# Performance work log

Hardware: AMD Instinct MI355X
Metric: run time of the kernel (lower is better)

Reference implementation:

```python
import jax, jax.numpy as jnp
import numpy as np

P = 16          # patch size
NH = 12         # num heads
DH = 64         # head dim
C = 768         # embed dim
DEPTH = 12
HID = 3072      # mlp hidden = 4*C
EPS = 1e-6


def _ln(x, g, b):
    m = x.mean(-1, keepdims=True)
    v = ((x - m) ** 2).mean(-1, keepdims=True)
    return (x - m) / jnp.sqrt(v + EPS) * g + b


def _rope_tables(seq_len, dim):
    inv_freq = 1.0 / (10000.0 ** (jnp.arange(0, dim, 2, dtype=jnp.float32) / dim))
    freqs = jnp.arange(seq_len, dtype=jnp.float32)[:, None] * inv_freq[None, :]  # [S, dim/2]
    emb = jnp.concatenate([freqs, freqs], axis=-1)  # [S, dim] (concat layout, as in source)
    return jnp.cos(emb), jnp.sin(emb)


def _apply_rope(q, k, cos, sin):
    def rot(t):  # interleaved rotate-half, exactly as torch source
        t1, t2 = t[..., ::2], t[..., 1::2]
        return jnp.stack([-t2, t1], axis=-1).reshape(t.shape)
    return q * cos + rot(q) * sin, k * cos + rot(k) * sin


def setup_inputs() -> dict:
    key = jax.random.key(0)
    ks = jax.random.split(key, 16)
    w = lambda k, shp: (jax.random.normal(k, shp, dtype=jnp.float32) * 0.02)
    inp = {
        "x": jax.random.normal(ks[0], (4, 6, 320, 320), dtype=jnp.float32),
        "conv_w": w(ks[1], (C, 3, P, P)),
        "conv_b": jnp.zeros((C,), jnp.float32),
        "ln1_g": jnp.ones((DEPTH, C), jnp.float32),
        "ln1_b": jnp.zeros((DEPTH, C), jnp.float32),
        "qkv_w": w(ks[2], (DEPTH, C, 3 * C)),
        "qkv_b": jnp.zeros((DEPTH, 3 * C), jnp.float32),
        "proj_w": w(ks[3], (DEPTH, C, C)),
        "proj_b": jnp.zeros((DEPTH, C), jnp.float32),
        "ln2_g": jnp.ones((DEPTH, C), jnp.float32),
        "ln2_b": jnp.zeros((DEPTH, C), jnp.float32),
        "fc1_w": w(ks[4], (DEPTH, C, HID)),
        "fc1_b": jnp.zeros((DEPTH, HID), jnp.float32),
        "fc2_w": w(ks[5], (DEPTH, HID, C)),
        "fc2_b": jnp.zeros((DEPTH, C), jnp.float32),
        "lnf_g": jnp.ones((C,), jnp.float32),
        "lnf_b": jnp.zeros((C,), jnp.float32),
    }
    return inp


def reference(x, conv_w, conv_b, ln1_g, ln1_b, qkv_w, qkv_b, proj_w, proj_b,
              ln2_g, ln2_b, fc1_w, fc1_b, fc2_w, fc2_b, lnf_g, lnf_b):
    B = x.shape[0]

    def embed(img):  # [B,3,H,W] -> [B, (H/P)*(W/P), C]
        y = jax.lax.conv_general_dilated(
            img, conv_w, window_strides=(P, P), padding="VALID",
            dimension_numbers=("NCHW", "OIHW", "NCHW")) + conv_b[None, :, None, None]
        b, c, hg, wg = y.shape
        return y.reshape(b, c, hg * wg).transpose(0, 2, 1)

    t = jnp.concatenate([embed(x[:, :3]), embed(x[:, 3:])], axis=1)  # [B,S,C], S=2*400=800
    S = t.shape[1]
    cos, sin = _rope_tables(S, DH)
    cos, sin = cos[None, None], sin[None, None]  # [1,1,S,DH]
    scale = DH ** -0.5

    def block(h, p):
        l1g, l1b, qw, qb, pw, pb, l2g, l2b, f1w, f1b, f2w, f2b = p
        y = _ln(h, l1g, l1b)
        qkv = (y @ qw + qb).reshape(B, S, 3, NH, DH).transpose(2, 0, 3, 1, 4)
        q, k, v = qkv[0], qkv[1], qkv[2]  # [B,NH,S,DH]
        q, k = _apply_rope(q, k, cos, sin)
        a = jax.nn.softmax(jnp.einsum("bhsd,bhtd->bhst", q, k) * scale, axis=-1)
        o = jnp.einsum("bhst,bhtd->bhsd", a, v).transpose(0, 2, 1, 3).reshape(B, S, C)
        h = h + (o @ pw + pb)
        y = _ln(h, l2g, l2b)
        h = h + (jax.nn.gelu(y @ f1w + f1b, approximate=False) @ f2w + f2b)
        return h, None

    params = (ln1_g, ln1_b, qkv_w, qkv_b, proj_w, proj_b,
              ln2_g, ln2_b, fc1_w, fc1_b, fc2_w, fc2_b)
    t, _ = jax.lax.scan(block, t, params)
    return _ln(t, lnf_g, lnf_b)
```

## Files before the change

### kernel.cpp

```cpp
#include <hip/hip_runtime.h>
#include <hip/hip_bf16.h>
#include <math.h>

#define S_LEN   800
#define SP_LEN  896
#define C_DIM   768
#define NHEAD   12
#define DHEAD   64
#define HID_DIM 3072
#define BATCH   4
#define NTOK    (BATCH * S_LEN)
#define DEPTH_N 12

using bf16x8 = __attribute__((ext_vector_type(8))) short;
using f32x4  = __attribute__((ext_vector_type(4))) float;

__device__ inline short f2bf(float x) {
    unsigned u = __builtin_bit_cast(unsigned, x);
    u += 0x7fff + ((u >> 16) & 1);
    return (short)(u >> 16);
}
__device__ inline float bf2f(short x) {
    unsigned u = ((unsigned)(unsigned short)x) << 16;
    return __builtin_bit_cast(float, u);
}

typedef const __attribute__((address_space(1))) void* gas_ptr;
typedef __attribute__((address_space(3))) void* las_ptr;
__device__ inline void async_copy16(const void* g, void* l) {
    __builtin_amdgcn_global_load_lds((gas_ptr)g, (las_ptr)l, 16, 0, 0);
}

__global__ __launch_bounds__(256)
void transpose_convert_kernel(const float* __restrict__ W, short* __restrict__ Wt,
                              int K, int N) {
    __shared__ float tile[32][33];
    int k0 = blockIdx.y * 32, n0 = blockIdx.x * 32;
    int tx = threadIdx.x & 31, ty = threadIdx.x >> 5;
#pragma unroll
    for (int i = ty; i < 32; i += 8)
        tile[i][tx] = W[(size_t)(k0 + i) * N + n0 + tx];
    __syncthreads();
#pragma unroll
    for (int i = ty; i < 32; i += 8)
        Wt[(size_t)(n0 + i) * K + k0 + tx] = f2bf(tile[tx][i]);
}

__global__ void convert_bf_kernel(const float* __restrict__ a, short* __restrict__ o, int n) {
    int i = blockIdx.x * 256 + threadIdx.x;
    if (i < n) o[i] = f2bf(a[i]);
}

__global__ void im2col_kernel(const float* __restrict__ x, short* __restrict__ A) {
    int idx = blockIdx.x * 256 + threadIdx.x;
    if (idx >= NTOK * 768) return;
    int kk = idx % 768;
    int s  = (idx / 768) % S_LEN;
    int b  = idx / (768 * S_LEN);
    int c  = kk / 256;
    int i  = (kk / 16) % 16;
    int j  = kk % 16;
    int half = s / 400, ss = s % 400;
    int hg = ss / 20, wg = ss % 20;
    int ch = half * 3 + c;
    A[idx] = f2bf(x[((size_t)(b * 6 + ch) * 320 + hg * 16 + i) * 320 + wg * 16 + j]);
}

template <int BN, bool GELU, bool RES, bool OBF>
__global__ __launch_bounds__(256)
void gemm_mfma(const short* __restrict__ A, const short* __restrict__ Bt,
               const float* __restrict__ bias, const float* __restrict__ res,
               void* __restrict__ Cout, int M, int N, int K) {
    constexpr int BM = 128, BK = 64;
    constexpr int TI = (BN == 128) ? 4 : 2;
    constexpr int TJ = 4;
    constexpr int ACALLS = BM * BK / (8 * 64);
    constexpr int BCALLS = BN * BK / (8 * 64);

    __shared__ __align__(16) short As[BM * BK];
    __shared__ __align__(16) short Bs[BN * BK];

    int tid = threadIdx.x;
    int w = tid >> 6, lane = tid & 63;
    int m0 = blockIdx.y * BM, n0 = blockIdx.x * BN;

    int wr = (BN == 128) ? (w >> 1) * 64 : w * 32;
    int wc = (BN == 128) ? (w & 1) * 64 : 0;

    f32x4 acc[TI][TJ];
#pragma unroll
    for (int i = 0; i < TI; ++i)
#pragma unroll
        for (int j = 0; j < TJ; ++j)
            acc[i][j] = (f32x4){0.f, 0.f, 0.f, 0.f};

    int lc = lane & 15, lq = lane >> 4;

    for (int k0 = 0; k0 < K; k0 += BK) {
#pragma unroll
        for (int j = w; j < ACALLS; j += 4) {
            int c = j * 64 + lane;
            int row = c >> 3, p = c & 7, q = p ^ (row & 7);
            async_copy16(A + (size_t)(m0 + row) * K + k0 + q * 8, As + j * 512);
        }
#pragma unroll
        for (int j = w; j < BCALLS; j += 4) {
            int c = j * 64 + lane;
            int row = c >> 3, p = c & 7, q = p ^ (row & 7);
            async_copy16(Bt + (size_t)(n0 + row) * K + k0 + q * 8, Bs + j * 512);
        }
        __syncthreads();

#pragma unroll
        for (int h = 0; h < 2; ++h) {
            bf16x8 afrag[TI], bfrag[TJ];
#pragma unroll
            for (int i = 0; i < TI; ++i) {
                int row = wr + i * 16 + lc;
                afrag[i] = *(const bf16x8*)(As + row * 64 + ((((h << 2) | lq)) ^ (row & 7)) * 8);
            }
#pragma unroll
            for (int j = 0; j < TJ; ++j) {
                int col = wc + j * 16 + lc;
                bfrag[j] = *(const bf16x8*)(Bs + col * 64 + ((((h << 2) | lq)) ^ (col & 7)) * 8);
            }
#pragma unroll
            for (int i = 0; i < TI; ++i)
#pragma unroll
                for (int j = 0; j < TJ; ++j)
                    acc[i][j] = __builtin_amdgcn_mfma_f32_16x16x32_bf16(
                        afrag[i], bfrag[j], acc[i][j], 0, 0, 0);
        }
        __syncthreads();
    }

    int rbase = lq * 4;
#pragma unroll
    for (int i = 0; i < TI; ++i)
#pragma unroll
        for (int j = 0; j < TJ; ++j)
#pragma unroll
            for (int r = 0; r < 4; ++r) {
                int m = m0 + wr + i * 16 + rbase + r;
                int n = n0 + wc + j * 16 + lc;
                float v = acc[i][j][r] + bias[n];
                if (RES) v += res[(size_t)m * N + n];
                if (GELU) v = 0.5f * v * (1.0f + erff(v * 0.70710678118654752f));
                if (OBF) ((short*)Cout)[(size_t)m * N + n] = f2bf(v);
                else     ((float*)Cout)[(size_t)m * N + n] = v;
            }
}

template <bool OBF>
__global__ __launch_bounds__(256)
void ln_kernel(const float* __restrict__ x, const float* __restrict__ g,
               const float* __restrict__ bta, void* __restrict__ yv) {
    int row = blockIdx.x;
    const float* xr = x + (size_t)row * C_DIM;
    int tid = threadIdx.x;

    float v0 = xr[tid], v1 = xr[tid + 256], v2 = xr[tid + 512];
    float s  = v0 + v1 + v2;
    float sq = v0 * v0 + v1 * v1 + v2 * v2;
#pragma unroll
    for (int off = 32; off; off >>= 1) {
        s  += __shfl_down(s, off);
        sq += __shfl_down(sq, off);
    }
    __shared__ float red1[4], red2[4];
    __shared__ float mean_s, rstd_s;
    int wv = tid / 64, lane = tid % 64;
    if (lane == 0) { red1[wv] = s; red2[wv] = sq; }
    __syncthreads();
    if (tid == 0) {
        float S1 = red1[0] + red1[1] + red1[2] + red1[3];
        float S2 = red2[0] + red2[1] + red2[2] + red2[3];
        float m = S1 / (float)C_DIM;
        float var = S2 / (float)C_DIM - m * m;
        mean_s = m;
        rstd_s = rsqrtf(var + 1e-6f);
    }
    __syncthreads();
    float m = mean_s, r = rstd_s;
    float o0 = (v0 - m) * r * g[tid]       + bta[tid];
    float o1 = (v1 - m) * r * g[tid + 256] + bta[tid + 256];
    float o2 = (v2 - m) * r * g[tid + 512] + bta[tid + 512];
    if (OBF) {
        short* yr = (short*)yv + (size_t)row * C_DIM;
        yr[tid] = f2bf(o0); yr[tid + 256] = f2bf(o1); yr[tid + 512] = f2bf(o2);
    } else {
        float* yr = (float*)yv + (size_t)row * C_DIM;
        yr[tid] = o0; yr[tid + 256] = o1; yr[tid + 512] = o2;
    }
}

__global__ __launch_bounds__(256)
void rope_qkv_kernel(const short* __restrict__ qkv, short* __restrict__ qb,
                     short* __restrict__ kb, short* __restrict__ vtb) {
    int st = blockIdx.x;
    int bh = blockIdx.y;
    int b = bh / NHEAD, h = bh % NHEAD;
    int s0 = st * 64;

    __shared__ __align__(16) short vlds[64][72];

    int tid = threadIdx.x;
    int sl = tid >> 2;
    int dc = (tid & 3) * 16;
    int s = s0 + sl;

    short qo[16], ko[16];
    if (s < S_LEN) {
        const short* base = qkv + ((size_t)(b * S_LEN + s)) * (3 * C_DIM) + h * DHEAD + dc;
        short qsh[16], ksh[16], vsh[16];
        *(bf16x8*)(qsh)     = *(const bf16x8*)(base);
        *(bf16x8*)(qsh + 8) = *(const bf16x8*)(base + 8);
        *(bf16x8*)(ksh)     = *(const bf16x8*)(base + C_DIM);
        *(bf16x8*)(ksh + 8) = *(const bf16x8*)(base + C_DIM + 8);
        *(bf16x8*)(vsh)     = *(const bf16x8*)(base + 2 * C_DIM);
        *(bf16x8*)(vsh + 8) = *(const bf16x8*)(base + 2 * C_DIM + 8);
        float qv[16], kv[16];
#pragma unroll
        for (int i = 0; i < 16; ++i) { qv[i] = bf2f(qsh[i]); kv[i] = bf2f(ksh[i]); }
#pragma unroll
        for (int i = 0; i < 16; ++i) {
            int d = dc + i;
            float ang = (float)s * exp2f(-(float)(d & 31) * 0.41524101186092029f);
            float c = cosf(ang), sn = sinf(ang);
            float sign = (i & 1) ? 1.0f : -1.0f;
            qo[i] = f2bf((qv[i] * c + sign * qv[i ^ 1] * sn) * 0.18033688011112042f);
            ko[i] = f2bf(kv[i] * c + sign * kv[i ^ 1] * sn);
        }
        *(bf16x8*)&vlds[sl][dc]     = *(bf16x8*)(vsh);
        *(bf16x8*)&vlds[sl][dc + 8] = *(bf16x8*)(vsh + 8);
    } else {
#pragma unroll
        for (int i = 0; i < 16; ++i) { qo[i] = 0; ko[i] = 0; vlds[sl][dc + i] = 0; }
    }
    {
        short* qd = qb + ((size_t)bh * SP_LEN + s) * DHEAD + dc;
        short* kd = kb + ((size_t)bh * SP_LEN + s) * DHEAD + dc;
        *(bf16x8*)(qd)     = *(bf16x8*)(qo);
        *(bf16x8*)(qd + 8) = *(bf16x8*)(qo + 8);
        *(bf16x8*)(kd)     = *(bf16x8*)(ko);
        *(bf16x8*)(kd + 8) = *(bf16x8*)(ko + 8);
    }
    __syncthreads();
    {
        int dr = tid >> 2, sc = (tid & 3) * 16;
        short vo[16];
#pragma unroll
        for (int i = 0; i < 16; ++i) vo[i] = vlds[sc + i][dr];
        short* vd = vtb + ((size_t)bh * DHEAD + dr) * SP_LEN + s0 + sc;
        *(bf16x8*)(vd)     = *(bf16x8*)(vo);
        *(bf16x8*)(vd + 8) = *(bf16x8*)(vo + 8);
    }
}

__global__ __launch_bounds__(256)
void attn_mfma_kernel(const short* __restrict__ qb, const short* __restrict__ kb,
                      const short* __restrict__ vtb, short* __restrict__ o) {
    int qt = blockIdx.x;
    int bh = blockIdx.y;
    int b = bh / NHEAD, h = bh % NHEAD;
    int m0 = qt * 64;

    __shared__ __align__(16) short Qs[64 * 64];
    __shared__ __align__(16) short Ks[128 * 64];
    __shared__ __align__(16) short Vts[64 * 128];
    __shared__ __align__(16) short Ps[64 * 136];

    int tid = threadIdx.x;
    int w = tid >> 6, lane = tid & 63;
    int lc = lane & 15, lq = lane >> 4;
    int kq = lq * 8;

    const short* qbase = qb + (size_t)bh * SP_LEN * DHEAD;
    const short* kbase = kb + (size_t)bh * SP_LEN * DHEAD;
    const short* vbase = vtb + (size_t)bh * DHEAD * SP_LEN;

    f32x4 oacc[4];
#pragma unroll
    for (int t = 0; t < 4; ++t) oacc[t] = (f32x4){0.f, 0.f, 0.f, 0.f};
    float mrow[4] = {-3.0e38f, -3.0e38f, -3.0e38f, -3.0e38f};
    float lrow[4] = {0.f, 0.f, 0.f, 0.f};

#pragma unroll
    for (int j = w; j < 8; j += 4) {
        int c = j * 64 + lane;
        int row = c >> 3, p = c & 7, q = p ^ (row & 7);
        async_copy16(qbase + (size_t)(m0 + row) * DHEAD + q * 8, Qs + j * 512);
    }

    for (int it = 0; it < 7; ++it) {
        int kt = it * 128;
#pragma unroll
        for (int j = w; j < 16; j += 4) {
            int c = j * 64 + lane;
            int row = c >> 3, p = c & 7, q = p ^ (row & 7);
            async_copy16(kbase + (size_t)(kt + row) * DHEAD + q * 8, Ks + j * 512);
        }
#pragma unroll
        for (int j = w; j < 16; j += 4) {
            int c = j * 64 + lane;
            int d = c >> 4, p = c & 15, sq = p ^ (d & 15);
            async_copy16(vbase + (size_t)d * SP_LEN + kt + sq * 8, Vts + j * 512);
        }
        __syncthreads();

        int nt = (it < 6) ? 8 : 2;

        int qrow = w * 16 + lc;
        bf16x8 aq0 = *(const bf16x8*)(Qs + qrow * 64 + ((lq) ^ (qrow & 7)) * 8);
        bf16x8 aq1 = *(const bf16x8*)(Qs + qrow * 64 + ((4 | lq) ^ (qrow & 7)) * 8);

        f32x4 sacc[8];
        for (int t = 0; t < nt; ++t) {
            int kr = t * 16 + lc;
            bf16x8 bk0 = *(const bf16x8*)(Ks + kr * 64 + ((lq) ^ (kr & 7)) * 8);
            bf16x8 bk1 = *(const bf16x8*)(Ks + kr * 64 + ((4 | lq) ^ (kr & 7)) * 8);
            f32x4 z = (f32x4){0.f, 0.f, 0.f, 0.f};
            z = __builtin_amdgcn_mfma_f32_16x16x32_bf16(aq0, bk0, z, 0, 0, 0);
            z = __builtin_amdgcn_mfma_f32_16x16x32_bf16(aq1, bk1, z, 0, 0, 0);
            sacc[t] = z;
        }

        float rmax[4];
#pragma unroll
        for (int r = 0; r < 4; ++r) {
            float m = sacc[0][r];
            for (int t = 1; t < nt; ++t) m = fmaxf(m, sacc[t][r]);
            rmax[r] = m;
        }
#pragma unroll
        for (int off = 1; off < 16; off <<= 1)
#pragma unroll
            for (int r = 0; r < 4; ++r)
                rmax[r] = fmaxf(rmax[r], __shfl_xor(rmax[r], off));

        float alpha[4], rsum[4] = {0.f, 0.f, 0.f, 0.f};
#pragma unroll
        for (int r = 0; r < 4; ++r) {
            float mnew = fmaxf(mrow[r], rmax[r]);
            alpha[r] = exp2f(mrow[r] - mnew);
            mrow[r] = mnew;
        }
        for (int t = 0; t < nt; ++t) {
#pragma unroll
            for (int r = 0; r < 4; ++r) {
                float p = exp2f(sacc[t][r] - mrow[r]);
                rsum[r] += p;
                Ps[(w * 16 + lq * 4 + r) * 136 + t * 16 + lc] = f2bf(p);
            }
        }
#pragma unroll
        for (int off = 1; off < 16; off <<= 1)
#pragma unroll
            for (int r = 0; r < 4; ++r)
                rsum[r] += __shfl_xor(rsum[r], off);
#pragma unroll
        for (int r = 0; r < 4; ++r) lrow[r] = lrow[r] * alpha[r] + rsum[r];
#pragma unroll
        for (int t = 0; t < 4; ++t)
#pragma unroll
            for (int r = 0; r < 4; ++r) oacc[t][r] *= alpha[r];

        int nk = (nt == 8) ? 4 : 1;
        for (int kstep = 0; kstep < nk; ++kstep) {
            bf16x8 ap = *(const bf16x8*)(Ps + (w * 16 + lc) * 136 + kstep * 32 + kq);
#pragma unroll
            for (int t = 0; t < 4; ++t) {
                int dr = t * 16 + lc;
                bf16x8 bv = *(const bf16x8*)(Vts + dr * 128 + ((((kstep << 2) | lq)) ^ (dr & 15)) * 8);
                oacc[t] = __builtin_amdgcn_mfma_f32_16x16x32_bf16(ap, bv, oacc[t], 0, 0, 0);
            }
        }
        __syncthreads();
    }

    float inv_l[4];
#pragma unroll
    for (int r = 0; r < 4; ++r) inv_l[r] = 1.0f / lrow[r];
#pragma unroll
    for (int t = 0; t < 4; ++t)
#pragma unroll
        for (int r = 0; r < 4; ++r) {
            int row = w * 16 + lq * 4 + r;
            int s = m0 + row;
            if (s < S_LEN) {
                int n = t * 16 + lc;
                o[((size_t)(b * S_LEN + s)) * C_DIM + h * DHEAD + n] = f2bf(oacc[t][r] * inv_l[r]);
            }
        }
}

extern "C" void kernel_launch(void* const* d_in, const int* in_sizes, int n_in,
                              void* d_out, int out_size, void* d_ws, size_t ws_size,
                              hipStream_t stream) {
    const float* x      = (const float*)d_in[0];
    const float* conv_w = (const float*)d_in[1];
    const float* conv_b = (const float*)d_in[2];
    const float* ln1_g  = (const float*)d_in[3];
    const float* ln1_b  = (const float*)d_in[4];
    const float* qkv_w  = (const float*)d_in[5];
    const float* qkv_b  = (const float*)d_in[6];
    const float* proj_w = (const float*)d_in[7];
    const float* proj_b = (const float*)d_in[8];
    const float* ln2_g  = (const float*)d_in[9];
    const float* ln2_b  = (const float*)d_in[10];
    const float* fc1_w  = (const float*)d_in[11];
    const float* fc1_b  = (const float*)d_in[12];
    const float* fc2_w  = (const float*)d_in[13];
    const float* fc2_b  = (const float*)d_in[14];
    const float* lnf_g  = (const float*)d_in[15];
    const float* lnf_b  = (const float*)d_in[16];

    const size_t NTC = (size_t)NTOK * C_DIM;
    const size_t HSD = (size_t)BATCH * NHEAD * SP_LEN * DHEAD;
    float* ws = (float*)d_ws;
    float* h       = ws;
    short* qkv_bf  = (short*)(h + NTC);
    short* qb      = qkv_bf + (size_t)NTOK * 3 * C_DIM;
    short* kb      = qb + HSD;
    short* vtb     = kb + HSD;
    short* y_bf    = vtb + HSD;
    short* big_bf  = y_bf + NTC;
    short* wbuf    = big_bf + (size_t)NTOK * HID_DIM;
    short* embed_wt = wbuf + (size_t)HID_DIM * C_DIM;

    convert_bf_kernel<<<(768 * 768 + 255) / 256, 256, 0, stream>>>(conv_w, embed_wt, 768 * 768);
    im2col_kernel<<<(NTOK * 768 + 255) / 256, 256, 0, stream>>>(x, big_bf);
    gemm_mfma<64, false, false, false><<<dim3(C_DIM / 64, NTOK / 128), 256, 0, stream>>>(
        big_bf, embed_wt, conv_b, nullptr, h, NTOK, C_DIM, C_DIM);

    for (int l = 0; l < DEPTH_N; ++l) {
        const float* l1g = ln1_g + (size_t)l * C_DIM;
        const float* l1b = ln1_b + (size_t)l * C_DIM;
        const float* qw  = qkv_w + (size_t)l * C_DIM * 3 * C_DIM;
        const float* qbs = qkv_b + (size_t)l * 3 * C_DIM;
        const float* pw  = proj_w + (size_t)l * C_DIM * C_DIM;
        const float* pb  = proj_b + (size_t)l * C_DIM;
        const float* l2g = ln2_g + (size_t)l * C_DIM;
        const float* l2b = ln2_b + (size_t)l * C_DIM;
        const float* f1w = fc1_w + (size_t)l * C_DIM * HID_DIM;
        const float* f1b = fc1_b + (size_t)l * HID_DIM;
        const float* f2w = fc2_w + (size_t)l * HID_DIM * C_DIM;
        const float* f2b = fc2_b + (size_t)l * C_DIM;

        ln_kernel<true><<<NTOK, 256, 0, stream>>>(h, l1g, l1b, y_bf);
        transpose_convert_kernel<<<dim3(3 * C_DIM / 32, C_DIM / 32), 256, 0, stream>>>(
            qw, wbuf, C_DIM, 3 * C_DIM);
        gemm_mfma<128, false, false, true><<<dim3(3 * C_DIM / 128, NTOK / 128), 256, 0, stream>>>(
            y_bf, wbuf, qbs, nullptr, qkv_bf, NTOK, 3 * C_DIM, C_DIM);

        rope_qkv_kernel<<<dim3(14, BATCH * NHEAD), 256, 0, stream>>>(qkv_bf, qb, kb, vtb);
        attn_mfma_kernel<<<dim3(13, BATCH * NHEAD), 256, 0, stream>>>(qb, kb, vtb, y_bf);

        transpose_convert_kernel<<<dim3(C_DIM / 32, C_DIM / 32), 256, 0, stream>>>(
            pw, wbuf, C_DIM, C_DIM);
        gemm_mfma<64, false, true, false><<<dim3(C_DIM / 64, NTOK / 128), 256, 0, stream>>>(
            y_bf, wbuf, pb, h, h, NTOK, C_DIM, C_DIM);

        ln_kernel<true><<<NTOK, 256, 0, stream>>>(h, l2g, l2b, y_bf);
        transpose_convert_kernel<<<dim3(HID_DIM / 32, C_DIM / 32), 256, 0, stream>>>(
            f1w, wbuf, C_DIM, HID_DIM);
        gemm_mfma<128, true, false, true><<<dim3(HID_DIM / 128, NTOK / 128), 256, 0, stream>>>(
            y_bf, wbuf, f1b, nullptr, big_bf, NTOK, HID_DIM, C_DIM);
        transpose_convert_kernel<<<dim3(C_DIM / 32, HID_DIM / 32), 256, 0, stream>>>(
            f2w, wbuf, HID_DIM, C_DIM);
        gemm_mfma<64, false, true, false><<<dim3(C_DIM / 64, NTOK / 128), 256, 0, stream>>>(
            big_bf, wbuf, f2b, h, h, NTOK, C_DIM, HID_DIM);
    }

    ln_kernel<false><<<NTOK, 256, 0, stream>>>(h, lnf_g, lnf_b, d_out);
}
```

Before: 2.803 ms.

## Add 256x256 pipelined MFMA GEMM for QKV/FC1 and batch weight transposes

Introduces a new 512-thread GEMM kernel with 256x256 output tiles, swizzled LDS layout, double-buffered async global-to-LDS loads and raised wave priority around the MFMA blocks. It is used for the QKV and FC1 projections to increase data reuse per tile. The four per-layer weight transpose/convert launches are merged into a single kernel writing to separate buffers, which removes launch overhead. In exchange, the large tiles give only about 117–156 blocks per GEMM, which may leave many CUs idle. The 128KB LDS use per block also limits occupancy, and the tail tile reads A rows past M, though those stores are guarded.

```diff
diff --git a/kernel.cpp b/kernel.cpp
--- a/kernel.cpp
+++ b/kernel.cpp
@@ -31,11 +31,17 @@
     __builtin_amdgcn_global_load_lds((gas_ptr)g, (las_ptr)l, 16, 0, 0);
 }
 
-__global__ __launch_bounds__(256)
-void transpose_convert_kernel(const float* __restrict__ W, short* __restrict__ Wt,
-                              int K, int N) {
+struct TP4 {
+    const float *qw, *pw, *f1, *f2;
+    short *wq, *wp, *w1, *w2;
+};
+
+template <int K, int N>
+__device__ __forceinline__ void tc_tile(const float* __restrict__ W,
+                                        short* __restrict__ Wt, int t) {
     __shared__ float tile[32][33];
-    int k0 = blockIdx.y * 32, n0 = blockIdx.x * 32;
+    int nb = t % (N / 32), kb = t / (N / 32);
+    int k0 = kb * 32, n0 = nb * 32;
     int tx = threadIdx.x & 31, ty = threadIdx.x >> 5;
 #pragma unroll
     for (int i = ty; i < 32; i += 8)
@@ -44,6 +50,15 @@
 #pragma unroll
     for (int i = ty; i < 32; i += 8)
         Wt[(size_t)(n0 + i) * K + k0 + tx] = f2bf(tile[tx][i]);
+}
+
+__global__ __launch_bounds__(256)
+void transpose4_kernel(TP4 p) {
+    int t = blockIdx.x;
+    if (t < 1728)          tc_tile<768, 2304>(p.qw, p.wq, t);
+    else if (t < 2304)     tc_tile<768, 768>(p.pw, p.wp, t - 1728);
+    else if (t < 4608)     tc_tile<768, 3072>(p.f1, p.w1, t - 2304);
+    else                   tc_tile<3072, 768>(p.f2, p.w2, t - 4608);
 }
 
 __global__ void convert_bf_kernel(const float* __restrict__ a, short* __restrict__ o, int n) {
@@ -148,6 +163,138 @@
                 if (GELU) v = 0.5f * v * (1.0f + erff(v * 0.70710678118654752f));
                 if (OBF) ((short*)Cout)[(size_t)m * N + n] = f2bf(v);
                 else     ((float*)Cout)[(size_t)m * N + n] = v;
+            }
+}
+
+template <bool GELU>
+__global__ __launch_bounds__(512, 2)
+void gemm256(const short* __restrict__ A, const short* __restrict__ Bt,
+             const float* __restrict__ bias, short* __restrict__ Cout,
+             int M, int N, int K) {
+    __shared__ __align__(16) short sm[65536];
+
+    const int tid = threadIdx.x;
+    const int w = tid >> 6, lane = tid & 63;
+    const int lc = lane & 15, lq = lane >> 4;
+    const int m0 = blockIdx.y * 256, n0 = blockIdx.x * 256;
+    const int wr = (w >> 2) * 128;
+    const int wc = (w & 3) * 64;
+
+    f32x4 acc[8][4];
+#pragma unroll
+    for (int i = 0; i < 8; ++i)
+#pragma unroll
+        for (int j = 0; j < 4; ++j) acc[i][j] = (f32x4){0.f, 0.f, 0.f, 0.f};
+
+    const int c0 = w * 64 + lane;
+    const int c1 = (8 + w) * 64 + lane;
+    const int row0 = c0 >> 2, row1 = c1 >> 2;
+    const int lqq0 = ((c0 & 3) - ((row0 & 7) >> 1)) & 3;
+    const int lqq1 = ((c1 & 3) - ((row1 & 7) >> 1)) & 3;
+    const int dst0 = w * 512;
+    const int dst1 = (8 + w) * 512;
+
+    int offA[8], offB[4];
+#pragma unroll
+    for (int i = 0; i < 8; ++i) {
+        int row = wr + i * 16 + lc, r = row & 7;
+        offA[i] = (row >> 3) * 256 + (r * 4 + ((lq + (r >> 1)) & 3)) * 8;
+    }
+#pragma unroll
+    for (int j = 0; j < 4; ++j) {
+        int col = wc + j * 16 + lc, r = col & 7;
+        offB[j] = (col >> 3) * 256 + (r * 4 + ((lq + (r >> 1)) & 3)) * 8;
+    }
+
+    const int NT = K >> 6;
+
+    auto stage = [&](int tsrc, int sel, int nb) {
+        int kk = sel >> 1;
+        const short* src = (sel & 1) ? Bt : A;
+        int brow = (sel & 1) ? n0 : m0;
+        short* dstp = sm + nb * 32768 + ((sel & 1) ? 16384 : 0) + kk * 8192;
+        int kbase = tsrc * 64 + kk * 32;
+        async_copy16(src + (size_t)(brow + row0) * K + kbase + lqq0 * 8, dstp + dst0);
+        async_copy16(src + (size_t)(brow + row1) * K + kbase + lqq1 * 8, dstp + dst1);
+    };
+
+#define MFMA16(J0, J1)                                                              \
+    _Pragma("unroll")                                                               \
+    for (int i = 0; i < 8; ++i) {                                                   \
+        acc[i][J0] = __builtin_amdgcn_mfma_f32_16x16x32_bf16(af[i], bfr[0],         \
+                                                             acc[i][J0], 0, 0, 0); \
+        acc[i][J1] = __builtin_amdgcn_mfma_f32_16x16x32_bf16(af[i], bfr[1],         \
+                                                             acc[i][J1], 0, 0, 0); \
+    }
+
+    stage(0, 0, 0); stage(0, 1, 0); stage(0, 2, 0); stage(0, 3, 0);
+    asm volatile("s_waitcnt vmcnt(4)" ::: "memory");
+    __builtin_amdgcn_s_barrier();
+
+    for (int t = 0; t < NT; ++t) {
+        const int nb = (t + 1) & 1;
+        const int tsrc = (t + 1 < NT) ? t + 1 : t;
+        const short* Abase = sm + (t & 1) * 32768;
+        const short* Bbase = Abase + 16384;
+        bf16x8 af[8], bfr[2];
+
+#pragma unroll
+        for (int i = 0; i < 8; ++i) af[i] = *(const bf16x8*)(Abase + offA[i]);
+        bfr[0] = *(const bf16x8*)(Bbase + offB[0]);
+        bfr[1] = *(const bf16x8*)(Bbase + offB[1]);
+        stage(tsrc, 0, nb);
+        __builtin_amdgcn_s_barrier();
+        __builtin_amdgcn_s_setprio(1);
+        MFMA16(0, 1)
+        __builtin_amdgcn_s_setprio(0);
+        __builtin_amdgcn_s_barrier();
+
+        bfr[0] = *(const bf16x8*)(Bbase + offB[2]);
+        bfr[1] = *(const bf16x8*)(Bbase + offB[3]);
+        stage(tsrc, 1, nb);
+        asm volatile("s_waitcnt vmcnt(4)" ::: "memory");
+        __builtin_amdgcn_s_barrier();
+        __builtin_amdgcn_s_setprio(1);
+        MFMA16(2, 3)
+        __builtin_amdgcn_s_setprio(0);
+        __builtin_amdgcn_s_barrier();
+
+#pragma unroll
+        for (int i = 0; i < 8; ++i) af[i] = *(const bf16x8*)(Abase + 8192 + offA[i]);
+        bfr[0] = *(const bf16x8*)(Bbase + 8192 + offB[0]);
+        bfr[1] = *(const bf16x8*)(Bbase + 8192 + offB[1]);
+        stage(tsrc, 2, nb);
+        __builtin_amdgcn_s_barrier();
+        __builtin_amdgcn_s_setprio(1);
+        MFMA16(0, 1)
+        __builtin_amdgcn_s_setprio(0);
+        __builtin_amdgcn_s_barrier();
+
+        bfr[0] = *(const bf16x8*)(Bbase + 8192 + offB[2]);
+        bfr[1] = *(const bf16x8*)(Bbase + 8192 + offB[3]);
+        stage(tsrc, 3, nb);
+        asm volatile("s_waitcnt vmcnt(4)" ::: "memory");
+        __builtin_amdgcn_s_barrier();
+        __builtin_amdgcn_s_setprio(1);
+        MFMA16(2, 3)
+        __builtin_amdgcn_s_setprio(0);
+        __builtin_amdgcn_s_barrier();
+    }
+#undef MFMA16
+
+#pragma unroll
+    for (int i = 0; i < 8; ++i)
+#pragma unroll
+        for (int j = 0; j < 4; ++j)
+#pragma unroll
+            for (int r = 0; r < 4; ++r) {
+                int m = m0 + wr + i * 16 + lq * 4 + r;
+                if (m < M) {
+                    int n = n0 + wc + j * 16 + lc;
+                    float v = acc[i][j][r] + bias[n];
+                    if (GELU) v = 0.5f * v * (1.0f + erff(v * 0.70710678118654752f));
+                    Cout[(size_t)m * N + n] = f2bf(v);
+                }
             }
 }
 
@@ -425,8 +572,11 @@
     short* vtb     = kb + HSD;
     short* y_bf    = vtb + HSD;
     short* big_bf  = y_bf + NTC;
-    short* wbuf    = big_bf + (size_t)NTOK * HID_DIM;
-    short* embed_wt = wbuf + (size_t)HID_DIM * C_DIM;
+    short* wq      = big_bf + (size_t)NTOK * HID_DIM;
+    short* wp      = wq + (size_t)3 * C_DIM * C_DIM;
+    short* w1      = wp + (size_t)C_DIM * C_DIM;
+    short* w2      = w1 + (size_t)C_DIM * HID_DIM;
+    short* embed_wt = w2 + (size_t)HID_DIM * C_DIM;
 
     convert_bf_kernel<<<(768 * 768 + 255) / 256, 256, 0, stream>>>(conv_w, embed_wt, 768 * 768);
     im2col_kernel<<<(NTOK * 768 + 255) / 256, 256, 0, stream>>>(x, big_bf);
@@ -447,29 +597,24 @@
         const float* f2w = fc2_w + (size_t)l * HID_DIM * C_DIM;
         const float* f2b = fc2_b + (size_t)l * C_DIM;
 
+        TP4 tp{qw, pw, f1w, f2w, wq, wp, w1, w2};
+        transpose4_kernel<<<6912, 256, 0, stream>>>(tp);
+
         ln_kernel<true><<<NTOK, 256, 0, stream>>>(h, l1g, l1b, y_bf);
-        transpose_convert_kernel<<<dim3(3 * C_DIM / 32, C_DIM / 32), 256, 0, stream>>>(
-            qw, wbuf, C_DIM, 3 * C_DIM);
-        gemm_mfma<128, false, false, true><<<dim3(3 * C_DIM / 128, NTOK / 128), 256, 0, stream>>>(
-            y_bf, wbuf, qbs, nullptr, qkv_bf, NTOK, 3 * C_DIM, C_DIM);
+        gemm256<false><<<dim3(3 * C_DIM / 256, (NTOK + 255) / 256), 512, 0, stream>>>(
+            y_bf, wq, qbs, qkv_bf, NTOK, 3 * C_DIM, C_DIM);
 
         rope_qkv_kernel<<<dim3(14, BATCH * NHEAD), 256, 0, stream>>>(qkv_bf, qb, kb, vtb);
         attn_mfma_kernel<<<dim3(13, BATCH * NHEAD), 256, 0, stream>>>(qb, kb, vtb, y_bf);
 
-        transpose_convert_kernel<<<dim3(C_DIM / 32, C_DIM / 32), 256, 0, stream>>>(
-            pw, wbuf, C_DIM, C_DIM);
         gemm_mfma<64, false, true, false><<<dim3(C_DIM / 64, NTOK / 128), 256, 0, stream>>>(
-            y_bf, wbuf, pb, h, h, NTOK, C_DIM, C_DIM);
+            y_bf, wp, pb, h, h, NTOK, C_DIM, C_DIM);
 
         ln_kernel<true><<<NTOK, 256, 0, stream>>>(h, l2g, l2b, y_bf);
-        transpose_convert_kernel<<<dim3(HID_DIM / 32, C_DIM / 32), 256, 0, stream>>>(
-            f1w, wbuf, C_DIM, HID_DIM);
-        gemm_mfma<128, true, false, true><<<dim3(HID_DIM / 128, NTOK / 128), 256, 0, stream>>>(
-            y_bf, wbuf, f1b, nullptr, big_bf, NTOK, HID_DIM, C_DIM);
-        transpose_convert_kernel<<<dim3(C_DIM / 32, HID_DIM / 32), 256, 0, stream>>>(
-            f2w, wbuf, HID_DIM, C_DIM);
+        gemm256<true><<<dim3(HID_DIM / 256, (NTOK + 255) / 256), 512, 0, stream>>>(
+            y_bf, w1, f1b, big_bf, NTOK, HID_DIM, C_DIM);
         gemm_mfma<64, false, true, false><<<dim3(C_DIM / 64, NTOK / 128), 256, 0, stream>>>(
-            big_bf, wbuf, f2b, h, h, NTOK, C_DIM, HID_DIM);
+            big_bf, w2, f2b, h, h, NTOK, C_DIM, HID_DIM);
     }
 
     ln_kernel<false><<<NTOK, 256, 0, stream>>>(h, lnf_g, lnf_b, d_out);
```

New measurement: 3.242 ms. 1.16x slower.
